# Optimization experiments

Measured on AMD Instinct MI355X. Metric: run time of the kernel, lower is better.

The kernel has to match this reference:

```python
import jax, jax.numpy as jnp
import numpy as np

B, Q, H = 1, 2048, 2048
NH, NKV, HD = 16, 8, 128
PAST = 2048
EPS = 1e-6


def rotate_half(x):
    x1, x2 = x[..., : x.shape[-1] // 2], x[..., x.shape[-1] // 2 :]
    return jnp.concatenate((-x2, x1), axis=-1)


def rms_norm(x, w, eps=EPS):
    var = jnp.mean(jnp.square(x.astype(jnp.float32)), axis=-1, keepdims=True)
    return (x * jax.lax.rsqrt(var + eps)) * w


def setup_inputs() -> dict:
    key = jax.random.key(0)
    ks = jax.random.split(key, 8)
    hidden_states = jax.random.normal(ks[0], (B, Q, H), jnp.float32)
    # RoPE tables for positions [PAST, PAST+Q)
    inv_freq = 1.0 / (1000000.0 ** (np.arange(0, HD, 2, dtype=np.float32) / HD))
    pos = np.arange(PAST, PAST + Q, dtype=np.float32)
    freqs = np.outer(pos, inv_freq)  # [Q, HD/2]
    emb = np.concatenate([freqs, freqs], axis=-1)  # [Q, HD]
    cos = jnp.asarray(np.cos(emb))[None].repeat(B, 0)
    sin = jnp.asarray(np.sin(emb))[None].repeat(B, 0)
    # causal additive mask over kv_len = PAST + Q
    q_idx = np.arange(Q)[:, None] + PAST
    kv_idx = np.arange(PAST + Q)[None, :]
    mask = np.where(kv_idx <= q_idx, 0.0, -1e9).astype(np.float32)
    attention_mask = jnp.asarray(mask)[None, None]  # [1,1,Q,PAST+Q]
    s = 1.0 / np.sqrt(H)
    return {
        "hidden_states": hidden_states,
        "cos": cos,
        "sin": sin,
        "attention_mask": attention_mask,
        "past_key": jax.random.normal(ks[1], (B, NKV, PAST, HD), jnp.float32),
        "past_value": jax.random.normal(ks[2], (B, NKV, PAST, HD), jnp.float32),
        "Wq": jax.random.normal(ks[3], (NH * HD, H), jnp.float32) * s,
        "Wk": jax.random.normal(ks[4], (NKV * HD, H), jnp.float32) * s,
        "Wv": jax.random.normal(ks[5], (NKV * HD, H), jnp.float32) * s,
        "Wo": jax.random.normal(ks[6], (NH * HD, NH * HD), jnp.float32) * s,
        "q_norm_w": jnp.ones((HD,), jnp.float32),
        "k_norm_w": jnp.ones((HD,), jnp.float32),
    }


def reference(hidden_states, cos, sin, attention_mask, past_key, past_value,
              Wq, Wk, Wv, Wo, q_norm_w, k_norm_w):
    bsz, q_len, _ = hidden_states.shape
    scaling = HD ** -0.5
    n_rep = NH // NKV

    q = jnp.einsum("bsh,dh->bsd", hidden_states, Wq).reshape(bsz, q_len, NH, HD).transpose(0, 2, 1, 3)
    k = jnp.einsum("bsh,dh->bsd", hidden_states, Wk).reshape(bsz, q_len, NKV, HD).transpose(0, 2, 1, 3)
    v = jnp.einsum("bsh,dh->bsd", hidden_states, Wv).reshape(bsz, q_len, NKV, HD).transpose(0, 2, 1, 3)

    q = rms_norm(q, q_norm_w)
    k = rms_norm(k, k_norm_w)

    c = cos[:, None]  # [B,1,Q,HD]
    s = sin[:, None]
    q = q * c + rotate_half(q) * s
    k = k * c + rotate_half(k) * s

    k_all = jnp.concatenate([past_key, k], axis=2)    # [B,NKV,PAST+Q,HD]
    v_all = jnp.concatenate([past_value, v], axis=2)
    new_key = k_all[:, :, -q_len:, :]
    new_value = v_all[:, :, -q_len:, :]

    kv_len = k_all.shape[2]
    k_rep = jnp.broadcast_to(k_all[:, :, None], (bsz, NKV, n_rep, kv_len, HD)).reshape(bsz, NH, kv_len, HD)
    v_rep = jnp.broadcast_to(v_all[:, :, None], (bsz, NKV, n_rep, kv_len, HD)).reshape(bsz, NH, kv_len, HD)

    scores = jnp.einsum("bhqd,bhkd->bhqk", q, k_rep) * scaling + attention_mask
    probs = jax.nn.softmax(scores.astype(jnp.float32), axis=-1).astype(q.dtype)
    out = jnp.einsum("bhqk,bhkd->bhqd", probs, v_rep)
    out = out.transpose(0, 2, 1, 3).reshape(bsz, q_len, NH * HD)
    out = jnp.einsum("bsd,hd->bsh", out, Wo)
    return out, new_key, new_value
```

## Files before the change

kernel.cpp:

```cpp
#include <hip/hip_runtime.h>
#include <hip/hip_bf16.h>

typedef __bf16 bf16_t;
typedef __bf16 bf16x8 __attribute__((ext_vector_type(8)));
typedef float f32x4 __attribute__((ext_vector_type(4)));

#define NH 16
#define NKV 8
#define HD 128
#define QLEN 2048
#define PASTLEN 2048
#define KVLEN 4096
#define NKOFF 4194304UL
#define NVOFF 6291456UL
#define SM_C1 0.12751741f
#define SM_C2 (-28.853900817779268f)

__device__ __forceinline__ void async16(const void* g, void* l) {
  __builtin_amdgcn_global_load_lds(
      (const __attribute__((address_space(1))) unsigned int*)g,
      (__attribute__((address_space(3))) unsigned int*)l, 16, 0, 0);
}

__device__ __forceinline__ bool detect_f32(const void* qw) {
  return *(const unsigned*)qw == 0x3F800000u;
}

__device__ __forceinline__ float ld1(const void* p, size_t i, bool f32) {
  return f32 ? ((const float*)p)[i] : (float)((const bf16_t*)p)[i];
}
__device__ __forceinline__ void st1(void* p, size_t i, bool f32, float v) {
  if (f32) ((float*)p)[i] = v; else ((bf16_t*)p)[i] = (bf16_t)v;
}
template <bool F32>
__device__ __forceinline__ uint4 ld8cvt(const void* p, size_t i) {
  if constexpr (!F32) {
    return *(const uint4*)((const bf16_t*)p + i);
  } else {
    const float* f = (const float*)p + i;
    float4 f0 = *(const float4*)f;
    float4 f1 = *(const float4*)(f + 4);
    union { bf16_t h[8]; uint4 u; } r;
    r.h[0] = (bf16_t)f0.x; r.h[1] = (bf16_t)f0.y; r.h[2] = (bf16_t)f0.z; r.h[3] = (bf16_t)f0.w;
    r.h[4] = (bf16_t)f1.x; r.h[5] = (bf16_t)f1.y; r.h[6] = (bf16_t)f1.z; r.h[7] = (bf16_t)f1.w;
    return r.u;
  }
}
__device__ __forceinline__ unsigned bfbits(float v) {
  bf16_t h = (bf16_t)v;
  union { bf16_t h; unsigned short u; } x; x.h = h;
  return (unsigned)x.u;
}

__global__ __launch_bounds__(256) void k_cvt4(
    const float* __restrict__ s0, const float* __restrict__ s1,
    const float* __restrict__ s2, const float* __restrict__ s3,
    bf16_t* __restrict__ d0, bf16_t* __restrict__ d1,
    bf16_t* __restrict__ d2, bf16_t* __restrict__ d3,
    const void* __restrict__ qw)
{
  if (!detect_f32(qw)) return;
  const int ten = blockIdx.y;
  const float* s; bf16_t* d; size_t n;
  switch (ten) {
    case 0:  s = s0; d = d0; n = 4194304; break;
    case 1:  s = s1; d = d1; n = 4194304; break;
    case 2:  s = s2; d = d2; n = 2097152; break;
    default: s = s3; d = d3; n = 2097152; break;
  }
  const size_t i = ((size_t)blockIdx.x * 256 + threadIdx.x) * 8;
  if (i >= n) return;
  uint4 v = ld8cvt<true>(s, i);
  *(uint4*)(d + i) = v;
}

__global__ __launch_bounds__(512) void k_gemm_qkv(
    const void* __restrict__ hs, const void* __restrict__ Wq,
    const void* __restrict__ Wk, const void* __restrict__ Wv,
    const bf16_t* __restrict__ hsb, const bf16_t* __restrict__ Wqb,
    const bf16_t* __restrict__ Wkb, const bf16_t* __restrict__ Wvb,
    const void* __restrict__ cs, const void* __restrict__ sn,
    const void* __restrict__ qw, const void* __restrict__ kw,
    bf16_t* __restrict__ qb, bf16_t* __restrict__ kc, void* __restrict__ dout)
{
  __shared__ __align__(16) char smem[98304];
  bf16_t* As = (bf16_t*)smem;
  bf16_t* Bs = (bf16_t*)(smem + 65536);
  bf16_t* xsb  = (bf16_t*)smem;
  float*  rsum = (float*)(smem + 67584);

  const bool f = detect_f32(qw);
  const bf16_t* A = f ? hsb : (const bf16_t*)hs;
  const int bx = blockIdx.x, by = blockIdx.y;
  const bf16_t* B; int n0;
  if (bx < 16)      { B = f ? Wqb : (const bf16_t*)Wq; n0 = bx * 128; }
  else if (bx < 24) { B = f ? Wkb : (const bf16_t*)Wk; n0 = (bx - 16) * 128; }
  else              { B = f ? Wvb : (const bf16_t*)Wv; n0 = (bx - 24) * 128; }
  const int m0 = by * 256;

  const int tid = threadIdx.x, lane = tid & 63, w = tid >> 6;
  const int wm = w >> 1, wn = w & 1;
  const int qid = lane & 15, quad = lane >> 4;
  const int srow = tid >> 3, ssegp = tid & 7;

  f32x4 acc[4][4] = {};

  auto stA = [&](int kt, int c) {
    const int row = c * 64 + srow;
    async16(A + (size_t)(m0 + row) * 2048 + kt * 64 + ((ssegp ^ (row & 7)) * 8),
            As + (kt & 1) * 16384 + (size_t)(c * 512 + tid) * 8);
  };
  auto stB = [&](int kt, int c) {
    const int row = c * 64 + srow;
    async16(B + (size_t)(n0 + row) * 2048 + kt * 64 + ((ssegp ^ (row & 7)) * 8),
            Bs + (kt & 1) * 8192 + (size_t)(c * 512 + tid) * 8);
  };

  stA(0, 0); stA(0, 1); stA(0, 2); stA(0, 3); stB(0, 0); stB(0, 1);

  const int NT = 32;
  for (int kt = 0; kt < NT; kt++) {
    const bf16_t* Ab = As + (kt & 1) * 16384;
    const bf16_t* Bb = Bs + (kt & 1) * 8192;
    bf16x8 af[4], bf2[2];

    if (kt + 1 < NT) {
      stA(kt + 1, 0); stA(kt + 1, 1);
      asm volatile("s_waitcnt vmcnt(2)" ::: "memory");
    } else {
      asm volatile("s_waitcnt vmcnt(0)" ::: "memory");
    }
    __builtin_amdgcn_s_barrier();
#pragma unroll
    for (int i = 0; i < 4; i++) {
      const int row = wm * 64 + i * 16 + qid;
      af[i] = *(const bf16x8*)(Ab + (size_t)row * 64 + ((quad ^ (row & 7)) * 8));
    }
#pragma unroll
    for (int j = 0; j < 2; j++) {
      const int row = wn * 64 + j * 16 + qid;
      bf2[j] = *(const bf16x8*)(Bb + (size_t)row * 64 + ((quad ^ (row & 7)) * 8));
    }
    __builtin_amdgcn_s_setprio(1);
#pragma unroll
    for (int i = 0; i < 4; i++)
#pragma unroll
      for (int j = 0; j < 2; j++)
        acc[i][j] = __builtin_amdgcn_mfma_f32_16x16x32_bf16(af[i], bf2[j], acc[i][j], 0, 0, 0);
    __builtin_amdgcn_s_setprio(0);
    __builtin_amdgcn_s_barrier();

    if (kt + 1 < NT) { stA(kt + 1, 2); stA(kt + 1, 3); }
#pragma unroll
    for (int j = 0; j < 2; j++) {
      const int row = wn * 64 + (j + 2) * 16 + qid;
      bf2[j] = *(const bf16x8*)(Bb + (size_t)row * 64 + ((quad ^ (row & 7)) * 8));
    }
    __builtin_amdgcn_s_setprio(1);
#pragma unroll
    for (int i = 0; i < 4; i++)
#pragma unroll
      for (int j = 0; j < 2; j++)
        acc[i][j + 2] = __builtin_amdgcn_mfma_f32_16x16x32_bf16(af[i], bf2[j], acc[i][j + 2], 0, 0, 0);
    __builtin_amdgcn_s_setprio(0);
    __builtin_amdgcn_s_barrier();

    if (kt + 1 < NT) { stB(kt + 1, 0); stB(kt + 1, 1); }
#pragma unroll
    for (int i = 0; i < 4; i++) {
      const int row = wm * 64 + i * 16 + qid;
      af[i] = *(const bf16x8*)(Ab + (size_t)row * 64 + (((4 + quad) ^ (row & 7)) * 8));
    }
#pragma unroll
    for (int j = 0; j < 2; j++) {
      const int row = wn * 64 + j * 16 + qid;
      bf2[j] = *(const bf16x8*)(Bb + (size_t)row * 64 + (((4 + quad) ^ (row & 7)) * 8));
    }
    __builtin_amdgcn_s_setprio(1);
#pragma unroll
    for (int i = 0; i < 4; i++)
#pragma unroll
      for (int j = 0; j < 2; j++)
        acc[i][j] = __builtin_amdgcn_mfma_f32_16x16x32_bf16(af[i], bf2[j], acc[i][j], 0, 0, 0);
    __builtin_amdgcn_s_setprio(0);
    __builtin_amdgcn_s_barrier();

#pragma unroll
    for (int j = 0; j < 2; j++) {
      const int row = wn * 64 + (j + 2) * 16 + qid;
      bf2[j] = *(const bf16x8*)(Bb + (size_t)row * 64 + (((4 + quad) ^ (row & 7)) * 8));
    }
    __builtin_amdgcn_s_setprio(1);
#pragma unroll
    for (int i = 0; i < 4; i++)
#pragma unroll
      for (int j = 0; j < 2; j++)
        acc[i][j + 2] = __builtin_amdgcn_mfma_f32_16x16x32_bf16(af[i], bf2[j], acc[i][j + 2], 0, 0, 0);
    __builtin_amdgcn_s_setprio(0);
    __builtin_amdgcn_s_barrier();
  }

  if (bx >= 24) {
    const int h = bx - 24;
#pragma unroll
    for (int i = 0; i < 4; i++)
#pragma unroll
      for (int j = 0; j < 4; j++) {
        const int rl = wm * 64 + i * 16 + quad * 4;
        const int d  = wn * 64 + j * 16 + qid;
#pragma unroll
        for (int r = 0; r < 4; r++) {
          const int s = by * 256 + rl + r;
          st1(dout, NVOFF + ((size_t)h * QLEN + s) * HD + d, f, acc[i][j][r]);
        }
      }
    return;
  }

#pragma unroll
  for (int i = 0; i < 4; i++)
#pragma unroll
    for (int r = 0; r < 4; r++) {
      float v = 0.f;
#pragma unroll
      for (int j = 0; j < 4; j++) v += acc[i][j][r] * acc[i][j][r];
#pragma unroll
      for (int o = 1; o < 16; o <<= 1) v += __shfl_xor(v, o, 64);
      if (qid == 0) rsum[wn * 256 + wm * 64 + i * 16 + quad * 4 + r] = v;
    }
#pragma unroll
  for (int i = 0; i < 4; i++) {
    const int rlb = wm * 64 + i * 16 + quad * 4;
#pragma unroll
    for (int j = 0; j < 4; j++) {
      const int d = wn * 64 + j * 16 + qid;
      union { bf16_t h[4]; unsigned long long u; } px;
#pragma unroll
      for (int r = 0; r < 4; r++) px.h[r] = (bf16_t)acc[i][j][r];
      *(unsigned long long*)(xsb + (size_t)d * 264 + rlb) = px.u;
    }
  }
  __syncthreads();
  const void* wgt = (bx < 16) ? qw : kw;
#pragma unroll
  for (int i = 0; i < 4; i++) {
    const int rlb = wm * 64 + i * 16 + quad * 4;
    float inv[4];
#pragma unroll
    for (int r = 0; r < 4; r++)
      inv[r] = rsqrtf((rsum[rlb + r] + rsum[256 + rlb + r]) * (1.0f / 128.0f) + 1e-6f);
#pragma unroll
    for (int j = 0; j < 4; j++) {
      const int d = wn * 64 + j * 16 + qid;
      const float wv  = ld1(wgt, d, f);
      const float wvp = ld1(wgt, d ^ 64, f);
      union { bf16_t h[4]; unsigned long long u; } xp;
      xp.u = *(const unsigned long long*)(xsb + (size_t)(d ^ 64) * 264 + rlb);
#pragma unroll
      for (int r = 0; r < 4; r++) {
        const int s = by * 256 + rlb + r;
        const float x  = acc[i][j][r];
        const float y  = x * inv[r] * wv;
        const float yp = (float)xp.h[r] * inv[r] * wvp;
        const float cv = ld1(cs, (size_t)s * HD + d, f);
        const float sv = ld1(sn, (size_t)s * HD + d, f);
        const float o  = (d < 64) ? y * cv - yp * sv : y * cv + yp * sv;
        if (bx < 16) {
          qb[(size_t)s * 2048 + bx * HD + d] = (bf16_t)o;
        } else {
          const int hk = bx - 16;
          st1(dout, NKOFF + ((size_t)hk * QLEN + s) * HD + d, f, o);
          kc[((size_t)hk * KVLEN + PASTLEN + s) * HD + d] = (bf16_t)o;
        }
      }
    }
  }
}

template <int TM>
__device__ __forceinline__ void gemm_acc(
    const bf16_t* __restrict__ A, const bf16_t* __restrict__ B,
    int lda, int ldb, int m0, int n0, int K,
    bf16_t* __restrict__ As, bf16_t* __restrict__ Bs, f32x4 (*acc)[4])
{
  constexpr int MI   = TM / 32;
  constexpr int ACH  = TM / 32;
  constexpr int ABUF = TM * 64;

  const int tid  = threadIdx.x;
  const int lane = tid & 63;
  const int w    = tid >> 6;
  const int wm   = w >> 1, wn = w & 1;
  const int qid  = lane & 15, quad = lane >> 4;

  const int srow = tid >> 3, ssegp = tid & 7;

  auto stageA = [&](int kt, int buf) {
#pragma unroll
    for (int c = 0; c < ACH; c++) {
      const int row = c * 32 + srow;
      async16(A + (size_t)(m0 + row) * lda + kt * 64 + ((ssegp ^ (row & 7)) * 8),
              As + buf * ABUF + (size_t)(c * 256 + tid) * 8);
    }
  };
  auto stageB = [&](int kt, int buf) {
#pragma unroll
    for (int c = 0; c < 4; c++) {
      const int row = c * 32 + srow;
      async16(B + (size_t)(n0 + row) * ldb + kt * 64 + ((ssegp ^ (row & 7)) * 8),
              Bs + buf * 8192 + (size_t)(c * 256 + tid) * 8);
    }
  };

  stageA(0, 0); stageB(0, 0);
  const int NT = K >> 6;
  for (int kt = 0; kt < NT; kt++) {
    const int cur = kt & 1;
    if (kt + 1 < NT) {
      stageA(kt + 1, cur ^ 1);
      if constexpr (TM == 128) asm volatile("s_waitcnt vmcnt(4)" ::: "memory");
      else                     asm volatile("s_waitcnt vmcnt(2)" ::: "memory");
    } else {
      asm volatile("s_waitcnt vmcnt(0)" ::: "memory");
    }
    __builtin_amdgcn_s_barrier();

    {
      bf16x8 af[MI], bfr[4];
#pragma unroll
      for (int j = 0; j < 4; j++) {
        const int row = wn * 64 + j * 16 + qid;
        bfr[j] = *(const bf16x8*)(Bs + cur * 8192 + (size_t)row * 64 + ((quad ^ (row & 7)) * 8));
      }
#pragma unroll
      for (int i = 0; i < MI; i++) {
        const int row = wm * (TM / 2) + i * 16 + qid;
        af[i] = *(const bf16x8*)(As + cur * ABUF + (size_t)row * 64 + ((quad ^ (row & 7)) * 8));
      }
      __builtin_amdgcn_s_setprio(1);
#pragma unroll
      for (int i = 0; i < MI; i++)
#pragma unroll
        for (int j = 0; j < 4; j++)
          acc[i][j] = __builtin_amdgcn_mfma_f32_16x16x32_bf16(af[i], bfr[j], acc[i][j], 0, 0, 0);
      __builtin_amdgcn_s_setprio(0);
    }
    if (kt + 1 < NT) stageB(kt + 1, cur ^ 1);
    __builtin_amdgcn_s_barrier();

    {
      bf16x8 af[MI], bfr[4];
#pragma unroll
      for (int j = 0; j < 4; j++) {
        const int row = wn * 64 + j * 16 + qid;
        bfr[j] = *(const bf16x8*)(Bs + cur * 8192 + (size_t)row * 64 + (((4 + quad) ^ (row & 7)) * 8));
      }
#pragma unroll
      for (int i = 0; i < MI; i++) {
        const int row = wm * (TM / 2) + i * 16 + qid;
        af[i] = *(const bf16x8*)(As + cur * ABUF + (size_t)row * 64 + (((4 + quad) ^ (row & 7)) * 8));
      }
      __builtin_amdgcn_s_setprio(1);
#pragma unroll
      for (int i = 0; i < MI; i++)
#pragma unroll
        for (int j = 0; j < 4; j++)
          acc[i][j] = __builtin_amdgcn_mfma_f32_16x16x32_bf16(af[i], bfr[j], acc[i][j], 0, 0, 0);
      __builtin_amdgcn_s_setprio(0);
    }
    __builtin_amdgcn_s_barrier();
  }
}

__global__ __launch_bounds__(256) void k_gemm_o(
    const bf16_t* __restrict__ aout, const void* __restrict__ Wo,
    const bf16_t* __restrict__ Wob, void* __restrict__ dout,
    const void* __restrict__ qw)
{
  __shared__ __align__(16) char smem[49152];
  bf16_t* As = (bf16_t*)smem;
  bf16_t* Bs = (bf16_t*)(smem + 16384);
  const bool f = detect_f32(qw);
  const bf16_t* B = f ? Wob : (const bf16_t*)Wo;
  f32x4 acc[2][4] = {};
  gemm_acc<64>(aout, B, 2048, 2048, blockIdx.y * 64, blockIdx.x * 128, 2048, As, Bs, acc);

  const int tid = threadIdx.x, lane = tid & 63, w = tid >> 6;
  const int wm = w >> 1, wn = w & 1, qid = lane & 15, quad = lane >> 4;
#pragma unroll
  for (int i = 0; i < 2; i++)
#pragma unroll
    for (int j = 0; j < 4; j++) {
      const int rr = blockIdx.y * 64 + wm * 32 + i * 16 + quad * 4;
      const int cc = blockIdx.x * 128 + wn * 64 + j * 16 + qid;
#pragma unroll
      for (int r = 0; r < 4; r++)
        st1(dout, (size_t)(rr + r) * 2048 + cc, f, acc[i][j][r]);
    }
}

template <bool F>
__device__ __forceinline__ void prep_body(
    const void* __restrict__ pk, const void* __restrict__ pv,
    const void* __restrict__ dout,
    bf16_t* __restrict__ kc, bf16_t* __restrict__ vt,
    unsigned (*tile)[65])
{
  const int tid = threadIdx.x;
  const int hk = blockIdx.x >> 5, kvt = blockIdx.x & 31;
  const int kv0 = kvt * 128;

  if (kv0 < PASTLEN) {
    const size_t base = ((size_t)hk * PASTLEN + kv0) * HD;
    bf16_t* dst = kc + ((size_t)hk * KVLEN + kv0) * HD;
#pragma unroll
    for (int p = 0; p < 8; p++) {
      const int id = p * 256 + tid;
      const int r = id >> 4, c8 = (id & 15) * 8;
      uint4 vv = ld8cvt<F>(pk, base + (size_t)r * HD + c8);
      *(uint4*)(dst + (size_t)r * HD + c8) = vv;
    }
  }

  const void* src; size_t base;
  if (kv0 < PASTLEN) { src = pv;   base = ((size_t)hk * PASTLEN + kv0) * HD; }
  else               { src = dout; base = NVOFF + ((size_t)hk * QLEN + (kv0 - PASTLEN)) * HD; }
#pragma unroll
  for (int p = 0; p < 4; p++) {
    const int id = p * 256 + tid;
    const int r = id >> 4, e8 = (id & 15) * 8;
    if constexpr (!F) {
      uint4 a = *(const uint4*)((const bf16_t*)src + base + (size_t)(2 * r) * HD + e8);
      uint4 b = *(const uint4*)((const bf16_t*)src + base + (size_t)(2 * r + 1) * HD + e8);
      unsigned av[4] = {a.x, a.y, a.z, a.w}, bv[4] = {b.x, b.y, b.z, b.w};
#pragma unroll
      for (int q = 0; q < 4; q++) {
        tile[e8 + 2 * q][r]     = (av[q] & 0xffffu) | (bv[q] << 16);
        tile[e8 + 2 * q + 1][r] = (av[q] >> 16)     | (bv[q] & 0xffff0000u);
      }
    } else {
      const float* fa = (const float*)src + base + (size_t)(2 * r) * HD + e8;
      const float* fb = (const float*)src + base + (size_t)(2 * r + 1) * HD + e8;
#pragma unroll
      for (int e = 0; e < 8; e++)
        tile[e8 + e][r] = bfbits(fa[e]) | (bfbits(fb[e]) << 16);
    }
  }
  __syncthreads();
#pragma unroll
  for (int p = 0; p < 8; p++) {
    const int id = p * 256 + tid;
    const int e = id >> 4, c4 = (id & 15) * 4;
    uint4 wv;
    if (c4 & 8) {
      wv.x = tile[e][c4 + 2]; wv.y = tile[e][c4 + 3]; wv.z = tile[e][c4];     wv.w = tile[e][c4 + 1];
    } else {
      wv.x = tile[e][c4];     wv.y = tile[e][c4 + 1]; wv.z = tile[e][c4 + 2]; wv.w = tile[e][c4 + 3];
    }
    *(uint4*)(vt + ((size_t)hk * HD + e) * KVLEN + kv0 + c4 * 2) = wv;
  }
}
__global__ __launch_bounds__(256) void k_prep_kv(
    const void* __restrict__ pk, const void* __restrict__ pv,
    const void* __restrict__ dout,
    bf16_t* __restrict__ kc, bf16_t* __restrict__ vt,
    const float* __restrict__ Wo, bf16_t* __restrict__ Wob,
    const void* __restrict__ qw)
{
  __shared__ unsigned tile[128][65];
  const int bx = blockIdx.x;
  if (bx >= 256) {
    if (!detect_f32(qw)) return;
    const size_t i = ((size_t)(bx - 256) * 256 + threadIdx.x) * 8;
    uint4 v = ld8cvt<true>(Wo, i);
    *(uint4*)(Wob + i) = v;
    return;
  }
  if (detect_f32(qw)) prep_body<true>(pk, pv, dout, kc, vt, tile);
  else                prep_body<false>(pk, pv, dout, kc, vt, tile);
}

__global__ __launch_bounds__(256, 2) void k_attn(
    const bf16_t* __restrict__ qb, const bf16_t* __restrict__ kc,
    const bf16_t* __restrict__ vt, bf16_t* __restrict__ aout)
{
  __shared__ bf16_t ks[2][64 * 128];
  __shared__ bf16_t vs[2][128 * 64];
  __shared__ float  lsx[2][64];

  const int tid = threadIdx.x, lane = tid & 63, w = tid >> 6;
  const int qid = lane & 15, quad = lane >> 4;
  const int qg = w & 1;
  const int kh = w >> 1;
  const int bx = blockIdx.x;
  const int h  = ((bx & 7) << 1) | (bx >> 3);
  const int hk = h >> 1;
  const int by = blockIdx.y;
  const int qt = (by < 16) ? by : 47 - by;
  const int q0 = qt * 64;

  bf16x8 qf[2][4];
#pragma unroll
  for (int i = 0; i < 2; i++)
#pragma unroll
    for (int kst = 0; kst < 4; kst++)
      qf[i][kst] = *(const bf16x8*)(qb + (size_t)(q0 + qg * 32 + i * 16 + qid) * 2048
                                       + h * HD + kst * 32 + quad * 8);

  f32x4 Oacc[2][8] = {};
  float lsum[2] = {0.f, 0.f};

  const int J = quad >> 1;
  int bpa[4];
#pragma unroll
  for (int s = 0; s < 4; s++)
    bpa[s] = 4 * (qid + 16 * ((2 * quad + ((s >> 1) ^ J)) & 3));

  const bf16_t* kbase = kc + (size_t)hk * KVLEN * HD;
  const bf16_t* vbase = vt + (size_t)hk * HD * KVLEN;
  const int r16 = tid >> 4, ksg = tid & 15;
  const int r8  = tid >> 3, vsg = tid & 7;
  const int nt = qt + 33;

  auto stage = [&](int t, int buf) {
    const int kv0 = t * 64;
#pragma unroll
    for (int c = 0; c < 4; c++) {
      const int kr = c * 16 + r16;
      async16(kbase + (size_t)(kv0 + kr) * HD + ((ksg ^ (kr & 7)) * 8),
              &ks[buf][(size_t)(c * 256 + tid) * 8]);
    }
#pragma unroll
    for (int c = 0; c < 4; c++) {
      const int vr = c * 32 + r8;
      async16(vbase + (size_t)vr * KVLEN + kv0 + ((vsg ^ (vr & 7)) * 8),
              &vs[buf][(size_t)(c * 256 + tid) * 8]);
    }
  };

  stage(0, 0);

  for (int t = 0; t < nt; ++t) {
    const int cur = t & 1;
    if (t + 1 < nt) {
      stage(t + 1, cur ^ 1);
      asm volatile("s_waitcnt vmcnt(8)" ::: "memory");
    } else {
      asm volatile("s_waitcnt vmcnt(0)" ::: "memory");
    }
    __builtin_amdgcn_s_barrier();

    const bf16_t* ksb = ks[cur];
    const bf16_t* vsb = vs[cur];
    const int kv0 = t * 64;

    f32x4 sf[2][2] = {};
    __builtin_amdgcn_s_setprio(1);
#pragma unroll
    for (int kst = 0; kst < 4; kst++) {
      bf16x8 kf[2];
#pragma unroll
      for (int j = 0; j < 2; j++)
        kf[j] = *(const bf16x8*)(ksb + (size_t)((kh * 2 + j) * 16 + qid) * 128
                                     + (((kst * 4 + quad) * 8) ^ ((qid & 7) * 8)));
#pragma unroll
      for (int i = 0; i < 2; i++)
#pragma unroll
        for (int j = 0; j < 2; j++)
          sf[i][j] = __builtin_amdgcn_mfma_f32_16x16x32_bf16(kf[j], qf[i][kst], sf[i][j], 0, 0, 0);
    }
    __builtin_amdgcn_s_setprio(0);

    const bool lastt = (t == nt - 1);
    bf16x8 pf[2];
#pragma unroll
    for (int i = 0; i < 2; i++) {
      const int qglob = q0 + qg * 32 + i * 16 + qid + PASTLEN;
      float pr[2][4];
#pragma unroll
      for (int j = 0; j < 2; j++) {
        const int kvb = kv0 + kh * 32 + j * 16 + quad * 4;
#pragma unroll
        for (int r = 0; r < 4; r++) {
          float v = fmaf(sf[i][j][r], SM_C1, SM_C2);
          if (lastt && (kvb + r) > qglob) v = -1e9f;
          const float p = exp2f(v);
          lsum[i] += p;
          pr[j][r] = p;
        }
      }
      unsigned pk00, pk01, pk10, pk11;
      asm("v_cvt_pk_bf16_f32 %0, %1, %2" : "=v"(pk00) : "v"(pr[0][0]), "v"(pr[0][1]));
      asm("v_cvt_pk_bf16_f32 %0, %1, %2" : "=v"(pk01) : "v"(pr[0][2]), "v"(pr[0][3]));
      asm("v_cvt_pk_bf16_f32 %0, %1, %2" : "=v"(pk10) : "v"(pr[1][0]), "v"(pr[1][1]));
      asm("v_cvt_pk_bf16_f32 %0, %1, %2" : "=v"(pk11) : "v"(pr[1][2]), "v"(pr[1][3]));
      const bool qodd = (quad & 1) != 0;
      const unsigned reg0 = qodd ? pk10 : pk00;
      const unsigned reg1 = qodd ? pk11 : pk01;
      const unsigned reg2 = qodd ? pk00 : pk10;
      const unsigned reg3 = qodd ? pk01 : pk11;
      union { unsigned u[4]; bf16x8 v; } pu;
      pu.u[0] = (unsigned)__builtin_amdgcn_ds_bpermute(bpa[0], (int)reg0);
      pu.u[1] = (unsigned)__builtin_amdgcn_ds_bpermute(bpa[1], (int)reg1);
      pu.u[2] = (unsigned)__builtin_amdgcn_ds_bpermute(bpa[2], (int)reg2);
      pu.u[3] = (unsigned)__builtin_amdgcn_ds_bpermute(bpa[3], (int)reg3);
      pf[i] = pu.v;
    }

    __builtin_amdgcn_s_setprio(1);
#pragma unroll
    for (int n = 0; n < 8; n++) {
      bf16x8 vf = *(const bf16x8*)(vsb + (size_t)(n * 16 + qid) * 64
                                       + (((kh * 4 + quad) * 8) ^ ((qid & 7) * 8)));
      Oacc[0][n] = __builtin_amdgcn_mfma_f32_16x16x32_bf16(pf[0], vf, Oacc[0][n], 0, 0, 0);
      Oacc[1][n] = __builtin_amdgcn_mfma_f32_16x16x32_bf16(pf[1], vf, Oacc[1][n], 0, 0, 0);
    }
    __builtin_amdgcn_s_setprio(0);
    __builtin_amdgcn_s_barrier();
  }

#pragma unroll
  for (int i = 0; i < 2; i++) {
    lsum[i] += __shfl_xor(lsum[i], 16, 64);
    lsum[i] += __shfl_xor(lsum[i], 32, 64);
  }
  if (quad == 0) {
    lsx[kh][qg * 32 + qid]      = lsum[0];
    lsx[kh][qg * 32 + 16 + qid] = lsum[1];
  }
  float* Osc = (float*)ks;
  if (kh == 1) {
#pragma unroll
    for (int i = 0; i < 2; i++)
#pragma unroll
      for (int n = 0; n < 8; n++)
#pragma unroll
        for (int r = 0; r < 4; r++)
          Osc[(size_t)qg * 4096 + (i * 16 + quad * 4 + r) * 128 + n * 16 + qid] = Oacc[i][n][r];
  }
  __syncthreads();
  if (kh == 0) {
#pragma unroll
    for (int i = 0; i < 2; i++) {
      float invl[4];
#pragma unroll
      for (int r = 0; r < 4; r++) {
        const int qq = qg * 32 + i * 16 + quad * 4 + r;
        invl[r] = 1.0f / (lsx[0][qq] + lsx[1][qq]);
      }
#pragma unroll
      for (int n = 0; n < 8; n++)
#pragma unroll
        for (int r = 0; r < 4; r++) {
          const float ot = Oacc[i][n][r]
            + Osc[(size_t)qg * 4096 + (i * 16 + quad * 4 + r) * 128 + n * 16 + qid];
          const int row = q0 + qg * 32 + i * 16 + quad * 4 + r;
          aout[(size_t)row * 2048 + h * HD + n * 16 + qid] = (bf16_t)(ot * invl[r]);
        }
    }
  }
}

extern "C" void kernel_launch(void* const* d_in, const int* in_sizes, int n_in,
                              void* d_out, int out_size, void* d_ws, size_t ws_size,
                              hipStream_t stream) {
  const void* hs = d_in[0];
  const void* cs = d_in[1];
  const void* sn = d_in[2];
  const void* pk = d_in[4];
  const void* pv = d_in[5];
  const void* Wq = d_in[6];
  const void* Wk = d_in[7];
  const void* Wv = d_in[8];
  const void* Wo = d_in[9];
  const void* qw = d_in[10];
  const void* kw = d_in[11];

  char* ws = (char*)d_ws;
  bf16_t* qb   = (bf16_t*)(ws);
  bf16_t* kc   = (bf16_t*)(ws + (size_t)8  * 1024 * 1024);
  bf16_t* hsb  = (bf16_t*)(ws + (size_t)16 * 1024 * 1024);
  bf16_t* vt   = (bf16_t*)(ws + (size_t)16 * 1024 * 1024);
  bf16_t* Wqb  = (bf16_t*)(ws + (size_t)24 * 1024 * 1024);
  bf16_t* aout = (bf16_t*)(ws + (size_t)24 * 1024 * 1024);
  bf16_t* Wkb  = (bf16_t*)(ws + (size_t)32 * 1024 * 1024);
  bf16_t* Wvb  = (bf16_t*)(ws + (size_t)36 * 1024 * 1024);
  bf16_t* Wob  = (bf16_t*)(ws + (size_t)32 * 1024 * 1024);

  hipLaunchKernelGGL(k_cvt4, dim3(2048, 4), dim3(256), 0, stream,
                     (const float*)hs, (const float*)Wq, (const float*)Wk, (const float*)Wv,
                     hsb, Wqb, Wkb, Wvb, qw);
  hipLaunchKernelGGL(k_gemm_qkv, dim3(32, 8), dim3(512), 0, stream,
                     hs, Wq, Wk, Wv, hsb, Wqb, Wkb, Wvb, cs, sn, qw, kw, qb, kc, d_out);
  hipLaunchKernelGGL(k_prep_kv, dim3(2304), dim3(256), 0, stream,
                     pk, pv, d_out, kc, vt, (const float*)Wo, Wob, qw);
  hipLaunchKernelGGL(k_attn, dim3(16, 32), dim3(256), 0, stream, qb, kc, vt, aout);
  hipLaunchKernelGGL(k_gemm_o, dim3(16, 32), dim3(256), 0, stream, aout, Wo, Wob, d_out, qw);
}
```

Before: 346.5 us.

## Halve attention query tile and load V fragments directly from global

After: 448.5 us. 29.4% more time.

```diff
diff --git a/kernel.cpp b/kernel.cpp
--- a/kernel.cpp
+++ b/kernel.cpp
@@ -480,13 +480,12 @@
   else                prep_body<false>(pk, pv, dout, kc, vt, tile);
 }
 
-__global__ __launch_bounds__(256, 2) void k_attn(
+__global__ __launch_bounds__(256, 4) void k_attn(
     const bf16_t* __restrict__ qb, const bf16_t* __restrict__ kc,
     const bf16_t* __restrict__ vt, bf16_t* __restrict__ aout)
 {
   __shared__ bf16_t ks[2][64 * 128];
-  __shared__ bf16_t vs[2][128 * 64];
-  __shared__ float  lsx[2][64];
+  __shared__ float  lsx[2][32];
 
   const int tid = threadIdx.x, lane = tid & 63, w = tid >> 6;
   const int qid = lane & 15, quad = lane >> 4;
@@ -496,19 +495,17 @@
   const int h  = ((bx & 7) << 1) | (bx >> 3);
   const int hk = h >> 1;
   const int by = blockIdx.y;
-  const int qt = (by < 16) ? by : 47 - by;
-  const int q0 = qt * 64;
-
-  bf16x8 qf[2][4];
-#pragma unroll
-  for (int i = 0; i < 2; i++)
-#pragma unroll
-    for (int kst = 0; kst < 4; kst++)
-      qf[i][kst] = *(const bf16x8*)(qb + (size_t)(q0 + qg * 32 + i * 16 + qid) * 2048
-                                       + h * HD + kst * 32 + quad * 8);
-
-  f32x4 Oacc[2][8] = {};
-  float lsum[2] = {0.f, 0.f};
+  const int qt = (by < 32) ? by : 95 - by;
+  const int q0 = qt * 32;
+
+  bf16x8 qf[4];
+#pragma unroll
+  for (int kst = 0; kst < 4; kst++)
+    qf[kst] = *(const bf16x8*)(qb + (size_t)(q0 + qg * 16 + qid) * 2048
+                                  + h * HD + kst * 32 + quad * 8);
+
+  f32x4 Oacc[8] = {};
+  float lsum = 0.f;
 
   const int J = quad >> 1;
   int bpa[4];
@@ -519,8 +516,7 @@
   const bf16_t* kbase = kc + (size_t)hk * KVLEN * HD;
   const bf16_t* vbase = vt + (size_t)hk * HD * KVLEN;
   const int r16 = tid >> 4, ksg = tid & 15;
-  const int r8  = tid >> 3, vsg = tid & 7;
-  const int nt = qt + 33;
+  const int nt = (qt * 32 + 2143) >> 6;
 
   auto stage = [&](int t, int buf) {
     const int kv0 = t * 64;
@@ -530,12 +526,6 @@
       async16(kbase + (size_t)(kv0 + kr) * HD + ((ksg ^ (kr & 7)) * 8),
               &ks[buf][(size_t)(c * 256 + tid) * 8]);
     }
-#pragma unroll
-    for (int c = 0; c < 4; c++) {
-      const int vr = c * 32 + r8;
-      async16(vbase + (size_t)vr * KVLEN + kv0 + ((vsg ^ (vr & 7)) * 8),
-              &vs[buf][(size_t)(c * 256 + tid) * 8]);
-    }
   };
 
   stage(0, 0);
@@ -544,17 +534,16 @@
     const int cur = t & 1;
     if (t + 1 < nt) {
       stage(t + 1, cur ^ 1);
-      asm volatile("s_waitcnt vmcnt(8)" ::: "memory");
+      asm volatile("s_waitcnt vmcnt(4)" ::: "memory");
     } else {
       asm volatile("s_waitcnt vmcnt(0)" ::: "memory");
     }
     __builtin_amdgcn_s_barrier();
 
     const bf16_t* ksb = ks[cur];
-    const bf16_t* vsb = vs[cur];
     const int kv0 = t * 64;
 
-    f32x4 sf[2][2] = {};
+    f32x4 sf[2] = {};
     __builtin_amdgcn_s_setprio(1);
 #pragma unroll
     for (int kst = 0; kst < 4; kst++) {
@@ -564,100 +553,86 @@
         kf[j] = *(const bf16x8*)(ksb + (size_t)((kh * 2 + j) * 16 + qid) * 128
                                      + (((kst * 4 + quad) * 8) ^ ((qid & 7) * 8)));
 #pragma unroll
-      for (int i = 0; i < 2; i++)
-#pragma unroll
-        for (int j = 0; j < 2; j++)
-          sf[i][j] = __builtin_amdgcn_mfma_f32_16x16x32_bf16(kf[j], qf[i][kst], sf[i][j], 0, 0, 0);
+      for (int j = 0; j < 2; j++)
+        sf[j] = __builtin_amdgcn_mfma_f32_16x16x32_bf16(kf[j], qf[kst], sf[j], 0, 0, 0);
     }
     __builtin_amdgcn_s_setprio(0);
 
+    bf16x8 vf[8];
+#pragma unroll
+    for (int n = 0; n < 8; n++)
+      vf[n] = *(const bf16x8*)(vbase + (size_t)(n * 16 + qid) * KVLEN
+                                     + kv0 + kh * 32 + quad * 8);
+
     const bool lastt = (t == nt - 1);
-    bf16x8 pf[2];
-#pragma unroll
-    for (int i = 0; i < 2; i++) {
-      const int qglob = q0 + qg * 32 + i * 16 + qid + PASTLEN;
-      float pr[2][4];
-#pragma unroll
-      for (int j = 0; j < 2; j++) {
-        const int kvb = kv0 + kh * 32 + j * 16 + quad * 4;
-#pragma unroll
-        for (int r = 0; r < 4; r++) {
-          float v = fmaf(sf[i][j][r], SM_C1, SM_C2);
-          if (lastt && (kvb + r) > qglob) v = -1e9f;
-          const float p = exp2f(v);
-          lsum[i] += p;
-          pr[j][r] = p;
-        }
-      }
-      unsigned pk00, pk01, pk10, pk11;
-      asm("v_cvt_pk_bf16_f32 %0, %1, %2" : "=v"(pk00) : "v"(pr[0][0]), "v"(pr[0][1]));
-      asm("v_cvt_pk_bf16_f32 %0, %1, %2" : "=v"(pk01) : "v"(pr[0][2]), "v"(pr[0][3]));
-      asm("v_cvt_pk_bf16_f32 %0, %1, %2" : "=v"(pk10) : "v"(pr[1][0]), "v"(pr[1][1]));
-      asm("v_cvt_pk_bf16_f32 %0, %1, %2" : "=v"(pk11) : "v"(pr[1][2]), "v"(pr[1][3]));
-      const bool qodd = (quad & 1) != 0;
-      const unsigned reg0 = qodd ? pk10 : pk00;
-      const unsigned reg1 = qodd ? pk11 : pk01;
-      const unsigned reg2 = qodd ? pk00 : pk10;
-      const unsigned reg3 = qodd ? pk01 : pk11;
-      union { unsigned u[4]; bf16x8 v; } pu;
-      pu.u[0] = (unsigned)__builtin_amdgcn_ds_bpermute(bpa[0], (int)reg0);
-      pu.u[1] = (unsigned)__builtin_amdgcn_ds_bpermute(bpa[1], (int)reg1);
-      pu.u[2] = (unsigned)__builtin_amdgcn_ds_bpermute(bpa[2], (int)reg2);
-      pu.u[3] = (unsigned)__builtin_amdgcn_ds_bpermute(bpa[3], (int)reg3);
-      pf[i] = pu.v;
-    }
+    const int qglob = q0 + qg * 16 + qid + PASTLEN;
+    float pr[2][4];
+#pragma unroll
+    for (int j = 0; j < 2; j++) {
+      const int kvb = kv0 + kh * 32 + j * 16 + quad * 4;
+#pragma unroll
+      for (int r = 0; r < 4; r++) {
+        float v = fmaf(sf[j][r], SM_C1, SM_C2);
+        if (lastt && (kvb + r) > qglob) v = -1e9f;
+        const float p = exp2f(v);
+        lsum += p;
+        pr[j][r] = p;
+      }
+    }
+    unsigned pk00, pk01, pk10, pk11;
+    asm("v_cvt_pk_bf16_f32 %0, %1, %2" : "=v"(pk00) : "v"(pr[0][0]), "v"(pr[0][1]));
+    asm("v_cvt_pk_bf16_f32 %0, %1, %2" : "=v"(pk01) : "v"(pr[0][2]), "v"(pr[0][3]));
+    asm("v_cvt_pk_bf16_f32 %0, %1, %2" : "=v"(pk10) : "v"(pr[1][0]), "v"(pr[1][1]));
+    asm("v_cvt_pk_bf16_f32 %0, %1, %2" : "=v"(pk11) : "v"(pr[1][2]), "v"(pr[1][3]));
+    const bool qodd = (quad & 1) != 0;
+    const unsigned reg0 = qodd ? pk10 : pk00;
+    const unsigned reg1 = qodd ? pk11 : pk01;
+    const unsigned reg2 = qodd ? pk00 : pk10;
+    const unsigned reg3 = qodd ? pk01 : pk11;
+    union { unsigned u[4]; bf16x8 v; } pu;
+    pu.u[0] = (unsigned)__builtin_amdgcn_ds_bpermute(bpa[0], (int)reg0);
+    pu.u[1] = (unsigned)__builtin_amdgcn_ds_bpermute(bpa[1], (int)reg1);
+    pu.u[2] = (unsigned)__builtin_amdgcn_ds_bpermute(bpa[2], (int)reg2);
+    pu.u[3] = (unsigned)__builtin_amdgcn_ds_bpermute(bpa[3], (int)reg3);
+    const bf16x8 pf = pu.v;
 
     __builtin_amdgcn_s_setprio(1);
 #pragma unroll
-    for (int n = 0; n < 8; n++) {
-      bf16x8 vf = *(const bf16x8*)(vsb + (size_t)(n * 16 + qid) * 64
-                                       + (((kh * 4 + quad) * 8) ^ ((qid & 7) * 8)));
-      Oacc[0][n] = __builtin_amdgcn_mfma_f32_16x16x32_bf16(pf[0], vf, Oacc[0][n], 0, 0, 0);
-      Oacc[1][n] = __builtin_amdgcn_mfma_f32_16x16x32_bf16(pf[1], vf, Oacc[1][n], 0, 0, 0);
-    }
+    for (int n = 0; n < 8; n++)
+      Oacc[n] = __builtin_amdgcn_mfma_f32_16x16x32_bf16(pf, vf[n], Oacc[n], 0, 0, 0);
     __builtin_amdgcn_s_setprio(0);
     __builtin_amdgcn_s_barrier();
   }
 
-#pragma unroll
-  for (int i = 0; i < 2; i++) {
-    lsum[i] += __shfl_xor(lsum[i], 16, 64);
-    lsum[i] += __shfl_xor(lsum[i], 32, 64);
-  }
-  if (quad == 0) {
-    lsx[kh][qg * 32 + qid]      = lsum[0];
-    lsx[kh][qg * 32 + 16 + qid] = lsum[1];
-  }
+  lsum += __shfl_xor(lsum, 16, 64);
+  lsum += __shfl_xor(lsum, 32, 64);
+  if (quad == 0) lsx[kh][qg * 16 + qid] = lsum;
+
   float* Osc = (float*)ks;
   if (kh == 1) {
 #pragma unroll
-    for (int i = 0; i < 2; i++)
-#pragma unroll
-      for (int n = 0; n < 8; n++)
-#pragma unroll
-        for (int r = 0; r < 4; r++)
-          Osc[(size_t)qg * 4096 + (i * 16 + quad * 4 + r) * 128 + n * 16 + qid] = Oacc[i][n][r];
+    for (int n = 0; n < 8; n++)
+#pragma unroll
+      for (int r = 0; r < 4; r++)
+        Osc[(size_t)(qg * 16 + quad * 4 + r) * 128 + n * 16 + qid] = Oacc[n][r];
   }
   __syncthreads();
   if (kh == 0) {
-#pragma unroll
-    for (int i = 0; i < 2; i++) {
-      float invl[4];
+    float invl[4];
+#pragma unroll
+    for (int r = 0; r < 4; r++) {
+      const int qq = qg * 16 + quad * 4 + r;
+      invl[r] = 1.0f / (lsx[0][qq] + lsx[1][qq]);
+    }
+#pragma unroll
+    for (int n = 0; n < 8; n++)
 #pragma unroll
       for (int r = 0; r < 4; r++) {
-        const int qq = qg * 32 + i * 16 + quad * 4 + r;
-        invl[r] = 1.0f / (lsx[0][qq] + lsx[1][qq]);
-      }
-#pragma unroll
-      for (int n = 0; n < 8; n++)
-#pragma unroll
-        for (int r = 0; r < 4; r++) {
-          const float ot = Oacc[i][n][r]
-            + Osc[(size_t)qg * 4096 + (i * 16 + quad * 4 + r) * 128 + n * 16 + qid];
-          const int row = q0 + qg * 32 + i * 16 + quad * 4 + r;
-          aout[(size_t)row * 2048 + h * HD + n * 16 + qid] = (bf16_t)(ot * invl[r]);
-        }
-    }
+        const float ot = Oacc[n][r]
+          + Osc[(size_t)(qg * 16 + quad * 4 + r) * 128 + n * 16 + qid];
+        const int row = q0 + qg * 16 + quad * 4 + r;
+        aout[(size_t)row * 2048 + h * HD + n * 16 + qid] = (bf16_t)(ot * invl[r]);
+      }
   }
 }
 
@@ -694,6 +669,6 @@
                      hs, Wq, Wk, Wv, hsb, Wqb, Wkb, Wvb, cs, sn, qw, kw, qb, kc, d_out);
   hipLaunchKernelGGL(k_prep_kv, dim3(2304), dim3(256), 0, stream,
                      pk, pv, d_out, kc, vt, (const float*)Wo, Wob, qw);
-  hipLaunchKernelGGL(k_attn, dim3(16, 32), dim3(256), 0, stream, qb, kc, vt, aout);
+  hipLaunchKernelGGL(k_attn, dim3(16, 64), dim3(256), 0, stream, qb, kc, vt, aout);
   hipLaunchKernelGGL(k_gemm_o, dim3(16, 32), dim3(256), 0, stream, aout, Wo, Wob, d_out, qw);
 }
```
